# Optimization experiments

Hardware: AMD Instinct MI355X
Metric: run time of the kernel (lower is better)

The kernel has to match this reference:

```python
import jax, jax.numpy as jnp
import numpy as np


def setup_inputs() -> dict:
    key = jax.random.key(0)
    k0, k1, k2, k3, k4 = jax.random.split(key, 5)
    T, B, S, H = 32, 8192, 256, 128
    return {
        "states_batch": jax.random.normal(k0, (T, B, S), dtype=jnp.float32),
        "W1": jax.random.normal(k1, (T, S, H), dtype=jnp.float32) * (S ** -0.5),
        "b1": jax.random.normal(k2, (T, H), dtype=jnp.float32) * 0.01,
        "W2": jax.random.normal(k3, (T, H, 1), dtype=jnp.float32) * 0.01,
        "b2": jax.random.normal(k4, (T, 1), dtype=jnp.float32) * 0.01,
    }


def reference(states_batch, W1, b1, W2, b2):
    # [T,B,S] @ [T,S,H] -> [T,B,H], bias, SiLU
    h = jnp.einsum('tbs,tsh->tbh', states_batch, W1) + b1[:, None, :]
    h = jax.nn.silu(h)
    # [T,B,H] @ [T,H,1] -> [T,B,1], bias, squeeze -> [T,B]
    out = jnp.einsum('tbh,tho->tbo', h, W2) + b2[:, None, :]
    return out.squeeze(-1)
```

## Files before the change

kernel.cpp:

```cpp
#include <hip/hip_runtime.h>
#include <hip/hip_bf16.h>

typedef __attribute__((ext_vector_type(8))) short bf16x8;
typedef __attribute__((ext_vector_type(4))) float f32x4;

#define T_DIM 32
#define B_DIM 8192
#define S_DIM 256
#define H_DIM 128
#define BM    32
#define NCH   16
#define BLOCKS_PER_T 16

#define GLD_LDS16(gsrc, ldst)                                                  \
  __builtin_amdgcn_global_load_lds(                                            \
      (const __attribute__((address_space(1))) void*)(gsrc),                   \
      (__attribute__((address_space(3))) void*)(ldst), 16, 0, 0)

__device__ __forceinline__ uint32_t cvt_pk_bf16(float lo, float hi) {
  uint32_t r;
  asm("v_cvt_pk_bf16_f32 %0, %1, %2" : "=v"(r) : "v"(lo), "v"(hi));
  return r;
}

__global__ __launch_bounds__(256, 2) void cvar_mlp_kernel(
    const float* __restrict__ states, const float* __restrict__ W1,
    const float* __restrict__ b1, const float* __restrict__ W2,
    const float* __restrict__ b2, float* __restrict__ out)
{
  __shared__ __align__(16) float ldsA[2][BM * S_DIM];
  __shared__ float red[2][4][BM];

  const int tid  = threadIdx.x;
  const int wid  = tid >> 6;
  const int lane = tid & 63;
  const int l15  = lane & 15;
  const int lg   = lane >> 4;

  const int bidx = blockIdx.x;
  const int xcd  = bidx & 7;
  const int slot = bidx >> 3;
  const int t    = xcd * 4 + (slot >> 4);
  const int cg   = slot & 15;
  const int b0   = cg * (BM * NCH);

  const float*  Ag  = states + ((size_t)t * B_DIM + b0) * S_DIM;
  const float4* A4  = reinterpret_cast<const float4*>(Ag);
  const float*  W1g = W1 + (size_t)t * (S_DIM * H_DIM);

#pragma unroll
  for (int i = 0; i < 8; ++i) {
    const int rowt = i * 4 + wid;
    const int sg   = lane ^ (rowt & 7);
    GLD_LDS16(A4 + (size_t)0 * 2048 + rowt * 64 + sg,
              &ldsA[0][(i * 256 + wid * 64) * 4]);
  }

  bf16x8 bfr[2][8];
#pragma unroll
  for (int nloc = 0; nloc < 2; ++nloc) {
    const int ncol = (wid * 2 + nloc) * 16 + l15;
#pragma unroll
    for (int ks = 0; ks < 8; ++ks) {
      const int kbase = ks * 32 + lg * 8;
      float e[8];
#pragma unroll
      for (int j = 0; j < 8; ++j)
        e[j] = W1g[(size_t)(kbase + j) * H_DIM + ncol];
      union { uint32_t u[4]; bf16x8 v; } uu;
      uu.u[0] = cvt_pk_bf16(e[0], e[1]);
      uu.u[1] = cvt_pk_bf16(e[2], e[3]);
      uu.u[2] = cvt_pk_bf16(e[4], e[5]);
      uu.u[3] = cvt_pk_bf16(e[6], e[7]);
      bfr[nloc][ks] = uu.v;
    }
  }

  float b1c[2], w2c[2];
#pragma unroll
  for (int nloc = 0; nloc < 2; ++nloc) {
    const int col = (wid * 2 + nloc) * 16 + l15;
    b1c[nloc] = b1[(size_t)t * H_DIM + col];
    w2c[nloc] = W2[(size_t)t * H_DIM + col];
  }
  const float b2t = b2[t];
  float* outt = out + (size_t)t * B_DIM + b0;

  __syncthreads();

  for (int c = 0; c < NCH; ++c) {
    const int cur = c & 1;

    if (c + 1 < NCH) {
#pragma unroll
      for (int i = 0; i < 8; ++i) {
        const int rowt = i * 4 + wid;
        const int sg   = lane ^ (rowt & 7);
        GLD_LDS16(A4 + (size_t)(c + 1) * 2048 + rowt * 64 + sg,
                  &ldsA[cur ^ 1][(i * 256 + wid * 64) * 4]);
      }
    }

    f32x4 acc[2][2];
#pragma unroll
    for (int mt = 0; mt < 2; ++mt)
#pragma unroll
      for (int nloc = 0; nloc < 2; ++nloc)
        acc[mt][nloc] = (f32x4){0.f, 0.f, 0.f, 0.f};

#pragma unroll
    for (int mt = 0; mt < 2; ++mt) {
      const int r = mt * 16 + l15;
      const int m = r & 7;
      bf16x8 afr[8];
#pragma unroll
      for (int ks = 0; ks < 8; ++ks) {
        const int ga = ks * 8 + lg * 2;
        const float4 f0 = *reinterpret_cast<const float4*>(
            &ldsA[cur][r * S_DIM + ((ga    ) ^ m) * 4]);
        const float4 f1 = *reinterpret_cast<const float4*>(
            &ldsA[cur][r * S_DIM + ((ga + 1) ^ m) * 4]);
        union { uint32_t u[4]; bf16x8 v; } uu;
        uu.u[0] = cvt_pk_bf16(f0.x, f0.y);
        uu.u[1] = cvt_pk_bf16(f0.z, f0.w);
        uu.u[2] = cvt_pk_bf16(f1.x, f1.y);
        uu.u[3] = cvt_pk_bf16(f1.z, f1.w);
        afr[ks] = uu.v;
      }
#pragma unroll
      for (int ks = 0; ks < 8; ++ks) {
        acc[mt][0] = __builtin_amdgcn_mfma_f32_16x16x32_bf16(afr[ks], bfr[0][ks], acc[mt][0], 0, 0, 0);
        acc[mt][1] = __builtin_amdgcn_mfma_f32_16x16x32_bf16(afr[ks], bfr[1][ks], acc[mt][1], 0, 0, 0);
      }
    }

#pragma unroll
    for (int mt = 0; mt < 2; ++mt) {
      float part[4];
#pragma unroll
      for (int r = 0; r < 4; ++r) {
        float s = 0.f;
#pragma unroll
        for (int nloc = 0; nloc < 2; ++nloc) {
          const float h   = acc[mt][nloc][r] + b1c[nloc];
          const float sig = 1.f / (1.f + __expf(-h));
          s += h * sig * w2c[nloc];
        }
        s += __shfl_xor(s, 1);
        s += __shfl_xor(s, 2);
        s += __shfl_xor(s, 4);
        s += __shfl_xor(s, 8);
        part[r] = s;
      }
      if (l15 == 0) {
#pragma unroll
        for (int r = 0; r < 4; ++r)
          red[cur][wid][mt * 16 + lg * 4 + r] = part[r];
      }
    }

    __syncthreads();

    if (tid < BM) {
      const float o = red[cur][0][tid] + red[cur][1][tid] +
                      red[cur][2][tid] + red[cur][3][tid] + b2t;
      outt[c * BM + tid] = o;
    }
  }
}

extern "C" void kernel_launch(void* const* d_in, const int* in_sizes, int n_in,
                              void* d_out, int out_size, void* d_ws, size_t ws_size,
                              hipStream_t stream) {
  const float* states = (const float*)d_in[0];
  const float* W1     = (const float*)d_in[1];
  const float* b1     = (const float*)d_in[2];
  const float* W2     = (const float*)d_in[3];
  const float* b2     = (const float*)d_in[4];
  float* out          = (float*)d_out;

  const int grid = T_DIM * BLOCKS_PER_T;
  cvar_mlp_kernel<<<grid, 256, 0, stream>>>(states, W1, b1, W2, b2, out);
}
```

Measured before the change: 65.49 us.

## Deepen states prefetch to a 4-buffer ring with vmcnt-counted barriers

```diff
diff --git a/kernel.cpp b/kernel.cpp
--- a/kernel.cpp
+++ b/kernel.cpp
@@ -8,14 +8,9 @@
 #define B_DIM 8192
 #define S_DIM 256
 #define H_DIM 128
-#define BM    32
-#define NCH   16
+#define BM    16
+#define NCH   32
 #define BLOCKS_PER_T 16
-
-#define GLD_LDS16(gsrc, ldst)                                                  \
-  __builtin_amdgcn_global_load_lds(                                            \
-      (const __attribute__((address_space(1))) void*)(gsrc),                   \
-      (__attribute__((address_space(3))) void*)(ldst), 16, 0, 0)
 
 __device__ __forceinline__ uint32_t cvt_pk_bf16(float lo, float hi) {
   uint32_t r;
@@ -28,7 +23,7 @@
     const float* __restrict__ b1, const float* __restrict__ W2,
     const float* __restrict__ b2, float* __restrict__ out)
 {
-  __shared__ __align__(16) float ldsA[2][BM * S_DIM];
+  __shared__ __align__(16) float bufs[4][BM * S_DIM];
   __shared__ float red[2][4][BM];
 
   const int tid  = threadIdx.x;
@@ -44,108 +39,99 @@
   const int cg   = slot & 15;
   const int b0   = cg * (BM * NCH);
 
-  const float*  Ag  = states + ((size_t)t * B_DIM + b0) * S_DIM;
-  const float4* A4  = reinterpret_cast<const float4*>(Ag);
-  const float*  W1g = W1 + (size_t)t * (S_DIM * H_DIM);
+  const float* Ag  = states + ((size_t)t * B_DIM + b0) * S_DIM;
+  const f32x4* A4  = reinterpret_cast<const f32x4*>(Ag);
+  const float* W1g = W1 + (size_t)t * (S_DIM * H_DIM);
+  float*      outw = out + (size_t)t * B_DIM + b0;
 
-#pragma unroll
-  for (int i = 0; i < 8; ++i) {
-    const int rowt = i * 4 + wid;
-    const int sg   = lane ^ (rowt & 7);
-    GLD_LDS16(A4 + (size_t)0 * 2048 + rowt * 64 + sg,
-              &ldsA[0][(i * 256 + wid * 64) * 4]);
+#define DMA(c, q)                                                              \
+  _Pragma("unroll")                                                            \
+  for (int i = 0; i < 4; ++i) {                                                \
+    const int r = wid * 4 + i;                                                 \
+    __builtin_amdgcn_global_load_lds(                                          \
+        (const __attribute__((address_space(1))) void*)(                       \
+            A4 + (size_t)(c) * (BM * 64) + r * 64 + (lane ^ (r & 7))),         \
+        (__attribute__((address_space(3))) void*)&bufs[q][r * S_DIM], 16, 0, 0); \
   }
 
-  bf16x8 bfr[2][8];
+  DMA(0, 0);
+  DMA(1, 1);
+  DMA(2, 2);
+
+  const int ncol0 = wid * 32 + l15;
+  const int ncol1 = ncol0 + 16;
+  bf16x8 bfr0[8], bfr1[8];
 #pragma unroll
-  for (int nloc = 0; nloc < 2; ++nloc) {
-    const int ncol = (wid * 2 + nloc) * 16 + l15;
+  for (int ks = 0; ks < 8; ++ks) {
+    const int kbase = ks * 32 + lg * 8;
+    float e[8];
+#pragma unroll
+    for (int j = 0; j < 8; ++j)
+      e[j] = W1g[(size_t)(kbase + j) * H_DIM + ncol0];
+    union { uint32_t u[4]; bf16x8 v; } uu;
+    uu.u[0] = cvt_pk_bf16(e[0], e[1]);
+    uu.u[1] = cvt_pk_bf16(e[2], e[3]);
+    uu.u[2] = cvt_pk_bf16(e[4], e[5]);
+    uu.u[3] = cvt_pk_bf16(e[6], e[7]);
+    bfr0[ks] = uu.v;
+  }
+#pragma unroll
+  for (int ks = 0; ks < 8; ++ks) {
+    const int kbase = ks * 32 + lg * 8;
+    float e[8];
+#pragma unroll
+    for (int j = 0; j < 8; ++j)
+      e[j] = W1g[(size_t)(kbase + j) * H_DIM + ncol1];
+    union { uint32_t u[4]; bf16x8 v; } uu;
+    uu.u[0] = cvt_pk_bf16(e[0], e[1]);
+    uu.u[1] = cvt_pk_bf16(e[2], e[3]);
+    uu.u[2] = cvt_pk_bf16(e[4], e[5]);
+    uu.u[3] = cvt_pk_bf16(e[6], e[7]);
+    bfr1[ks] = uu.v;
+  }
+
+  const float b1c0 = b1[(size_t)t * H_DIM + ncol0];
+  const float b1c1 = b1[(size_t)t * H_DIM + ncol1];
+  const float w2c0 = W2[(size_t)t * H_DIM + ncol0];
+  const float w2c1 = W2[(size_t)t * H_DIM + ncol1];
+  const float b2t  = b2[t];
+
+  asm volatile("s_waitcnt vmcnt(0) lgkmcnt(0)\n\ts_barrier" ::: "memory");
+
+#pragma unroll 1
+  for (int c = 0; c < NCH; ++c) {
+    if (c + 3 < NCH) { DMA(c + 3, (c + 3) & 3); }
+
+    const float* buf = bufs[c & 3];
+    const int m7 = l15 & 7;
+    f32x4 acc0 = {0.f, 0.f, 0.f, 0.f};
+    f32x4 acc1 = {0.f, 0.f, 0.f, 0.f};
 #pragma unroll
     for (int ks = 0; ks < 8; ++ks) {
-      const int kbase = ks * 32 + lg * 8;
-      float e[8];
-#pragma unroll
-      for (int j = 0; j < 8; ++j)
-        e[j] = W1g[(size_t)(kbase + j) * H_DIM + ncol];
+      const int g = ks * 8 + lg * 2;
+      const f32x4 f0 = *reinterpret_cast<const f32x4*>(
+          &buf[l15 * S_DIM + ((g    ) ^ m7) * 4]);
+      const f32x4 f1 = *reinterpret_cast<const f32x4*>(
+          &buf[l15 * S_DIM + ((g + 1) ^ m7) * 4]);
       union { uint32_t u[4]; bf16x8 v; } uu;
-      uu.u[0] = cvt_pk_bf16(e[0], e[1]);
-      uu.u[1] = cvt_pk_bf16(e[2], e[3]);
-      uu.u[2] = cvt_pk_bf16(e[4], e[5]);
-      uu.u[3] = cvt_pk_bf16(e[6], e[7]);
-      bfr[nloc][ks] = uu.v;
-    }
-  }
-
-  float b1c[2], w2c[2];
-#pragma unroll
-  for (int nloc = 0; nloc < 2; ++nloc) {
-    const int col = (wid * 2 + nloc) * 16 + l15;
-    b1c[nloc] = b1[(size_t)t * H_DIM + col];
-    w2c[nloc] = W2[(size_t)t * H_DIM + col];
-  }
-  const float b2t = b2[t];
-  float* outt = out + (size_t)t * B_DIM + b0;
-
-  __syncthreads();
-
-  for (int c = 0; c < NCH; ++c) {
-    const int cur = c & 1;
-
-    if (c + 1 < NCH) {
-#pragma unroll
-      for (int i = 0; i < 8; ++i) {
-        const int rowt = i * 4 + wid;
-        const int sg   = lane ^ (rowt & 7);
-        GLD_LDS16(A4 + (size_t)(c + 1) * 2048 + rowt * 64 + sg,
-                  &ldsA[cur ^ 1][(i * 256 + wid * 64) * 4]);
-      }
+      uu.u[0] = cvt_pk_bf16(f0.x, f0.y);
+      uu.u[1] = cvt_pk_bf16(f0.z, f0.w);
+      uu.u[2] = cvt_pk_bf16(f1.x, f1.y);
+      uu.u[3] = cvt_pk_bf16(f1.z, f1.w);
+      acc0 = __builtin_amdgcn_mfma_f32_16x16x32_bf16(uu.v, bfr0[ks], acc0, 0, 0, 0);
+      acc1 = __builtin_amdgcn_mfma_f32_16x16x32_bf16(uu.v, bfr1[ks], acc1, 0, 0, 0);
     }
 
-    f32x4 acc[2][2];
-#pragma unroll
-    for (int mt = 0; mt < 2; ++mt)
-#pragma unroll
-      for (int nloc = 0; nloc < 2; ++nloc)
-        acc[mt][nloc] = (f32x4){0.f, 0.f, 0.f, 0.f};
-
-#pragma unroll
-    for (int mt = 0; mt < 2; ++mt) {
-      const int r = mt * 16 + l15;
-      const int m = r & 7;
-      bf16x8 afr[8];
-#pragma unroll
-      for (int ks = 0; ks < 8; ++ks) {
-        const int ga = ks * 8 + lg * 2;
-        const float4 f0 = *reinterpret_cast<const float4*>(
-            &ldsA[cur][r * S_DIM + ((ga    ) ^ m) * 4]);
-        const float4 f1 = *reinterpret_cast<const float4*>(
-            &ldsA[cur][r * S_DIM + ((ga + 1) ^ m) * 4]);
-        union { uint32_t u[4]; bf16x8 v; } uu;
-        uu.u[0] = cvt_pk_bf16(f0.x, f0.y);
-        uu.u[1] = cvt_pk_bf16(f0.z, f0.w);
-        uu.u[2] = cvt_pk_bf16(f1.x, f1.y);
-        uu.u[3] = cvt_pk_bf16(f1.z, f1.w);
-        afr[ks] = uu.v;
-      }
-#pragma unroll
-      for (int ks = 0; ks < 8; ++ks) {
-        acc[mt][0] = __builtin_amdgcn_mfma_f32_16x16x32_bf16(afr[ks], bfr[0][ks], acc[mt][0], 0, 0, 0);
-        acc[mt][1] = __builtin_amdgcn_mfma_f32_16x16x32_bf16(afr[ks], bfr[1][ks], acc[mt][1], 0, 0, 0);
-      }
-    }
-
-#pragma unroll
-    for (int mt = 0; mt < 2; ++mt) {
+    const int cb = c & 1;
+    {
       float part[4];
 #pragma unroll
       for (int r = 0; r < 4; ++r) {
-        float s = 0.f;
-#pragma unroll
-        for (int nloc = 0; nloc < 2; ++nloc) {
-          const float h   = acc[mt][nloc][r] + b1c[nloc];
-          const float sig = 1.f / (1.f + __expf(-h));
-          s += h * sig * w2c[nloc];
-        }
+        const float h0   = acc0[r] + b1c0;
+        const float h1   = acc1[r] + b1c1;
+        const float sig0 = 1.f / (1.f + __expf(-h0));
+        const float sig1 = 1.f / (1.f + __expf(-h1));
+        float s = h0 * sig0 * w2c0 + h1 * sig1 * w2c1;
         s += __shfl_xor(s, 1);
         s += __shfl_xor(s, 2);
         s += __shfl_xor(s, 4);
@@ -155,16 +141,22 @@
       if (l15 == 0) {
 #pragma unroll
         for (int r = 0; r < 4; ++r)
-          red[cur][wid][mt * 16 + lg * 4 + r] = part[r];
+          red[cb][wid][lg * 4 + r] = part[r];
       }
     }
 
-    __syncthreads();
+    if (c < NCH - 3) {
+      asm volatile("s_waitcnt vmcnt(8) lgkmcnt(0)\n\ts_barrier" ::: "memory");
+    } else if (c == NCH - 3) {
+      asm volatile("s_waitcnt vmcnt(4) lgkmcnt(0)\n\ts_barrier" ::: "memory");
+    } else {
+      asm volatile("s_waitcnt vmcnt(0) lgkmcnt(0)\n\ts_barrier" ::: "memory");
+    }
 
     if (tid < BM) {
-      const float o = red[cur][0][tid] + red[cur][1][tid] +
-                      red[cur][2][tid] + red[cur][3][tid] + b2t;
-      outt[c * BM + tid] = o;
+      const float o = red[cb][0][tid] + red[cb][1][tid] + red[cb][2][tid] +
+                      red[cb][3][tid] + b2t;
+      outw[c * BM + tid] = o;
     }
   }
 }
```

Result: slower. 74.29 us (+13.4%).
